# Kernel tuning notes

Hardware: AMD Instinct MI355X
Metric: run time of the kernel (lower is better)

Reference implementation:

```python
import jax, jax.numpy as jnp
import numpy as np

B, S, D, H = 4, 2048, 2048, 16
HD = D // H  # 128


def setup_inputs() -> dict:
    key = jax.random.key(0)
    k1, k2, k3 = jax.random.split(key, 3)
    sc = 1.0 / np.sqrt(D)
    return {
        "x": jax.random.normal(k1, (B, S, D), dtype=jnp.float32),
        "W_qkv": jax.random.normal(k2, (D, 3 * D), dtype=jnp.float32) * sc,
        "W_out": jax.random.normal(k3, (D, D), dtype=jnp.float32) * sc,
        "b_out": jnp.zeros((D,), dtype=jnp.float32),
    }


def _rotate_half(t):
    t1, t2 = jnp.split(t, 2, axis=-1)
    return jnp.concatenate([-t2, t1], axis=-1)


def reference(x, W_qkv, W_out, b_out):
    b, s, d = x.shape
    qkv = jnp.einsum('bsd,de->bse', x, W_qkv)  # fused QKV projection
    q, k, v = jnp.split(qkv, 3, axis=-1)
    # [b, h, s, hd]
    q = q.reshape(b, s, H, HD).transpose(0, 2, 1, 3)
    k = k.reshape(b, s, H, HD).transpose(0, 2, 1, 3)
    v = v.reshape(b, s, H, HD).transpose(0, 2, 1, 3)
    # RoPE (NeoX-style half-split), past_kv=None so positions = arange(s)
    pos = jnp.arange(s, dtype=jnp.float32)
    theta = 1.0 / (10000.0 ** (jnp.arange(0, HD, 2, dtype=jnp.float32) / HD))
    angles = pos[:, None] * theta[None, :]           # [s, hd/2]
    cos = jnp.concatenate([jnp.cos(angles)] * 2, -1)  # [s, hd] (repeat halves)
    sin = jnp.concatenate([jnp.sin(angles)] * 2, -1)
    cos = cos[None, None]  # [1,1,s,hd]
    sin = sin[None, None]
    q = q * cos + _rotate_half(q) * sin
    k = k * cos + _rotate_half(k) * sin
    # causal SDPA, scale = 1/sqrt(head_dim)
    scale = 1.0 / jnp.sqrt(jnp.asarray(HD, dtype=q.dtype))
    scores = jnp.einsum('bhqd,bhkd->bhqk', q, k) * scale
    causal = jnp.tril(jnp.ones((s, s), dtype=bool))
    scores = jnp.where(causal[None, None], scores, jnp.finfo(scores.dtype).min)
    attn = jax.nn.softmax(scores, axis=-1)
    out = jnp.einsum('bhqk,bhkd->bhqd', attn, v)
    out = out.transpose(0, 2, 1, 3).reshape(b, s, D)
    return jnp.einsum('bsd,de->bse', out, W_out) + b_out
```

## Files before the change

### kernel.cpp

```cpp
#include <hip/hip_runtime.h>

typedef unsigned short ushort_t;
typedef unsigned int u32;
typedef __attribute__((ext_vector_type(8))) short bf16x8;
typedef __attribute__((ext_vector_type(8))) unsigned short u16x8;
typedef __attribute__((ext_vector_type(4))) float f32x4;
typedef __attribute__((ext_vector_type(16))) float f32x16;

#define B_ 4
#define S_ 2048
#define D_ 2048
#define H_ 16
#define HD_ 128

__device__ __forceinline__ ushort_t f2bf(float f) {
  u32 x = __builtin_bit_cast(u32, f);
  x += 0x7fffu + ((x >> 16) & 1u);
  return (ushort_t)(x >> 16);
}
__device__ __forceinline__ float bf2f(ushort_t u) {
  u32 x = ((u32)u) << 16;
  return __builtin_bit_cast(float, x);
}

#define GLL16(srcp, ldsp)                                            \
  __builtin_amdgcn_global_load_lds(                                  \
      (const __attribute__((address_space(1))) u32*)(srcp),          \
      (__attribute__((address_space(3))) u32*)(ldsp), 16, 0, 0)

struct __align__(8) us4 { ushort_t x, y, z, w; };

__global__ void k_cvt_bf16(const float* __restrict__ in, ushort_t* __restrict__ out, int n) {
  int i = (blockIdx.x * 256 + threadIdx.x) * 4;
  if (i >= n) return;
  float4 v = *(const float4*)(in + i);
  us4 o;
  o.x = f2bf(v.x); o.y = f2bf(v.y); o.z = f2bf(v.z); o.w = f2bf(v.w);
  *(us4*)(out + i) = o;
}

__global__ void k_transpose_bf16(const float* __restrict__ in, ushort_t* __restrict__ out,
                                 int R, int C) {
  __shared__ float ld[32][33];
  int c0 = blockIdx.x * 32, r0 = blockIdx.y * 32;
  int tc = threadIdx.x & 31, tr = threadIdx.x >> 5;
#pragma unroll
  for (int i = 0; i < 4; ++i) {
    int r = tr + i * 8;
    ld[r][tc] = in[(size_t)(r0 + r) * C + c0 + tc];
  }
  __syncthreads();
#pragma unroll
  for (int i = 0; i < 4; ++i) {
    int r = tr + i * 8;
    out[(size_t)(c0 + r) * R + r0 + tc] = f2bf(ld[tc][r]);
  }
}

__global__ void k_rope_tables(float* __restrict__ cost, float* __restrict__ sint) {
  int i = blockIdx.x * 256 + threadIdx.x;
  int s = i >> 6, j = i & 63;
  double th = pow(10000.0, -(double)j / 64.0);
  double a = (double)s * th;
  cost[i] = (float)cos(a);
  sint[i] = (float)sin(a);
}

template <int MODE>
__global__ __launch_bounds__(512) void k_g8(const ushort_t* __restrict__ A,
                                            const ushort_t* __restrict__ Bt,
                                            void* __restrict__ Cout,
                                            const float* __restrict__ bias,
                                            ushort_t* __restrict__ VtB,
                                            int M, int N, int K) {
  __shared__ __attribute__((aligned(16))) ushort_t As[2][256 * 64];
  __shared__ __attribute__((aligned(16))) ushort_t Bs[2][256 * 64];
  const int tid = threadIdx.x;
  const int w = tid >> 6, l = tid & 63;
  const int l31 = l & 31, hl = l >> 5;
  const int wm = w >> 2, wn = w & 3;

  const int cpx = gridDim.x >> 3;
  const int bid = blockIdx.x;
  const int swzid = (bid & 7) * cpx + (bid >> 3);
  const int nbn = N >> 8;
  const size_t m0 = (size_t)(swzid / nbn) * 256;
  const size_t n0 = (size_t)(swzid % nbn) * 256;

  const size_t Kp = (size_t)K * 2;
  const char* Ab = (const char*)A + m0 * Kp;
  const char* Bb = (const char*)Bt + n0 * Kp;

  const int r0 = tid >> 3;
  const int ci16 = (tid & 7) * 16;
  const int sw0 = (((tid & 7) ^ (r0 & 7)) << 4);
  const int sw1 = (((tid & 7) ^ ((r0 + 64) & 7)) << 4);

#define STG_HALF(gbase, hrow, ldsbase, tcol)                                   \
  {                                                                            \
    GLL16((gbase) + (size_t)((hrow) + r0) * Kp + (tcol) + sw0,                 \
          (char*)(ldsbase) + ((hrow) + r0) * 128 + ci16);                      \
    GLL16((gbase) + (size_t)((hrow) + r0 + 64) * Kp + (tcol) + sw1,            \
          (char*)(ldsbase) + ((hrow) + r0 + 64) * 128 + ci16);                 \
  }

  f32x16 acc[4][2] = {};
  const int NI = K >> 7;

  const int arow = wm * 128 + l31;
  const int brow0 = wn * 64 + l31;

  STG_HALF(Ab, 0,   As[0], (size_t)0);
  STG_HALF(Ab, 128, As[0], (size_t)0);
  STG_HALF(Bb, 0,   Bs[0], (size_t)0);
  STG_HALF(Bb, 128, Bs[0], (size_t)0);
  STG_HALF(Bb, 0,   Bs[1], (size_t)128);
  STG_HALF(Bb, 128, Bs[1], (size_t)128);
  asm volatile("s_waitcnt vmcnt(4)");
  __builtin_amdgcn_sched_barrier(0);
  __builtin_amdgcn_s_barrier();

  for (int it = 0; it < NI; ++it) {
    const int t1 = 2 * it + 1;
    const bool more = (it + 1 < NI);
    const size_t cA1 = (size_t)t1 * 128;
    const size_t cT2 = (size_t)(t1 + 1) * 128;
    const size_t cT3 = (size_t)(t1 + 2) * 128;
    bf16x8 bq[2][4];
#pragma unroll
    for (int ph = 0; ph < 8; ++ph) {
      const int slot = ph >> 2;
      const int q = ph & 3;
      const char* Ac = (const char*)As[slot];
      const char* Bc = (const char*)Bs[slot];
      bf16x8 af[4];
      const int ar = arow + q * 32;
#pragma unroll
      for (int ks = 0; ks < 4; ++ks) {
        const int c = ks * 2 + hl;
        af[ks] = *(const bf16x8*)(Ac + ar * 128 + ((c ^ (ar & 7)) << 4));
      }
      if (q == 0) {
#pragma unroll
        for (int nt = 0; nt < 2; ++nt) {
          const int br = brow0 + nt * 32;
#pragma unroll
          for (int ks = 0; ks < 4; ++ks) {
            const int c = ks * 2 + hl;
            bq[nt][ks] = *(const bf16x8*)(Bc + br * 128 + ((c ^ (br & 7)) << 4));
          }
        }
      }
      if (ph == 0)      STG_HALF(Ab, 0,   As[1], cA1)
      else if (ph == 1) STG_HALF(Ab, 128, As[1], cA1)
      else if (ph == 2) { if (more) STG_HALF(Bb, 0,   Bs[0], cT2) }
      else if (ph == 3) { if (more) STG_HALF(Bb, 128, Bs[0], cT2) }
      else if (ph == 4) { if (more) STG_HALF(Ab, 0,   As[0], cT2) }
      else if (ph == 5) { if (more) STG_HALF(Ab, 128, As[0], cT2) }
      else if (ph == 6) { if (more) STG_HALF(Bb, 0,   Bs[1], cT3) }
      else              { if (more) STG_HALF(Bb, 128, Bs[1], cT3) }
      asm volatile("s_waitcnt lgkmcnt(0)");
      __builtin_amdgcn_sched_barrier(0);
      __builtin_amdgcn_s_setprio(1);
#pragma unroll
      for (int ks = 0; ks < 4; ++ks) {
        acc[q][0] = __builtin_amdgcn_mfma_f32_32x32x16_bf16(af[ks], bq[0][ks], acc[q][0], 0, 0, 0);
        acc[q][1] = __builtin_amdgcn_mfma_f32_32x32x16_bf16(af[ks], bq[1][ks], acc[q][1], 0, 0, 0);
      }
      __builtin_amdgcn_s_setprio(0);
      if (ph == 3) {
        if (more) asm volatile("s_waitcnt vmcnt(4)");
        else      asm volatile("s_waitcnt vmcnt(0)");
        __builtin_amdgcn_sched_barrier(0);
      } else if (ph == 7 && more) {
        asm volatile("s_waitcnt vmcnt(4)");
        __builtin_amdgcn_sched_barrier(0);
      }
      __builtin_amdgcn_s_barrier();
    }
  }

  if (MODE == 2) {
#pragma unroll
    for (int nt = 0; nt < 2; ++nt) {
      const size_t col = n0 + wn * 64 + nt * 32 + l31;
      const float bia = bias[col];
#pragma unroll
      for (int mt = 0; mt < 4; ++mt)
#pragma unroll
        for (int r = 0; r < 16; ++r) {
          const size_t row = m0 + wm * 128 + mt * 32 + (r & 3) + 8 * (r >> 2) + 4 * hl;
          ((float*)Cout)[row * N + col] = acc[mt][nt][r] + bia;
        }
    }
  } else {
    ushort_t* Qbase = (ushort_t*)Cout;
#pragma unroll
    for (int nt = 0; nt < 2; ++nt) {
      const int col = (int)n0 + wn * 64 + nt * 32 + l31;
      const int p3 = col >> 11, rem = col & 2047;
      const int h = rem >> 7, d = rem & 127;
      if (p3 < 2) {
        ushort_t* base = Qbase + (size_t)p3 * 16777216ull + (size_t)h * (S_ * HD_) + d;
#pragma unroll
        for (int mt = 0; mt < 4; ++mt)
#pragma unroll
          for (int r = 0; r < 16; ++r) {
            const int row = (int)m0 + wm * 128 + mt * 32 + (r & 3) + 8 * (r >> 2) + 4 * hl;
            const int b2 = row >> 11, s = row & 2047;
            base[(size_t)b2 * (H_ * S_ * HD_) + (size_t)s * HD_] = f2bf(acc[mt][nt][r]);
          }
      } else {
        ushort_t* baseV = VtB + ((size_t)h * HD_ + d) * S_;
#pragma unroll
        for (int mt = 0; mt < 4; ++mt)
#pragma unroll
          for (int r = 0; r < 16; ++r) {
            const int row = (int)m0 + wm * 128 + mt * 32 + (r & 3) + 8 * (r >> 2) + 4 * hl;
            const int b2 = row >> 11, s = row & 2047;
            baseV[(size_t)b2 * ((size_t)H_ * HD_ * S_) + s] = f2bf(acc[mt][nt][r]);
          }
      }
    }
  }
#undef STG_HALF
}

__global__ void k_rope2(ushort_t* __restrict__ Qr, ushort_t* __restrict__ Kr,
                        const float* __restrict__ cost, const float* __restrict__ sint,
                        float qs) {
  int s0 = blockIdx.x * 32, h = blockIdx.y, z = blockIdx.z;
  const bool isQ = (z < B_);
  const int b = isQ ? z : z - B_;
  const float sc = isQ ? qs : 1.0f;
  ushort_t* t8 = isQ ? Qr : Kr;
  int bh = b * H_ + h;
  const int t = threadIdx.x;
  const int sr = t >> 3, dj = (t & 7) * 8;
  const int s = s0 + sr;
  ushort_t* base = t8 + ((size_t)bh * S_ + s) * HD_;
  u16x8 lo = *(const u16x8*)(base + dj);
  u16x8 hi = *(const u16x8*)(base + 64 + dj);
  const float* cs = cost + s * 64 + dj;
  const float* sn = sint + s * 64 + dj;
  u16x8 olo, ohi;
#pragma unroll
  for (int j = 0; j < 8; ++j) {
    float fl = bf2f(lo[j]), fh = bf2f(hi[j]);
    float c = cs[j], sv = sn[j];
    olo[j] = f2bf((fl * c - fh * sv) * sc);
    ohi[j] = f2bf((fh * c + fl * sv) * sc);
  }
  *(u16x8*)(base + dj) = olo;
  *(u16x8*)(base + 64 + dj) = ohi;
}

__global__ __launch_bounds__(256, 2) void k_attn6(const ushort_t* __restrict__ Q,
                                                  const ushort_t* __restrict__ K,
                                                  const ushort_t* __restrict__ Vt,
                                                  ushort_t* __restrict__ O) {
  __shared__ __attribute__((aligned(16))) ushort_t Ks[2][64 * 128];
  __shared__ __attribute__((aligned(16))) ushort_t Vs[128 * 64];
  __shared__ __attribute__((aligned(16))) ushort_t Pl[8][16 * 72];

  const int id = blockIdx.x;
  const int work = (id & 7) * 128 + (id >> 3);
  const int bh = work >> 4;
  const int qt = 15 - (work & 15);
  const int b = bh >> 4, h = bh & 15;

  const int tid = threadIdx.x;
  const int w = tid >> 6, l = tid & 63;
  const int lr = l & 15, lg = l >> 4;
  const int qb = qt * 128 + w * 32;

  const ushort_t* Qp = Q + (size_t)bh * S_ * HD_;
  const char* Kpb = (const char*)(K + (size_t)bh * S_ * HD_);
  const char* Vpb = (const char*)(Vt + (size_t)bh * HD_ * S_);

  int kr[4], ksz[4], vr[4], vsz[4];
#pragma unroll
  for (int r = 0; r < 4; ++r) {
    int c = r * 256 + tid;
    kr[r] = c >> 4;
    ksz[r] = (((c & 15) ^ (kr[r] & 15)) << 4);
    vr[r] = c >> 3;
    vsz[r] = (((c & 7) ^ (vr[r] & 7)) << 4);
  }

#define STAGE_K(kb_, bufi)                                                       \
  {                                                                              \
    _Pragma("unroll") for (int r = 0; r < 4; ++r)                                \
        GLL16(Kpb + (size_t)((kb_) + kr[r]) * 256 + ksz[r],                      \
              (char*)Ks[bufi] + (size_t)(r * 256 + tid) * 16);                   \
  }
#define STAGE_V(kb_)                                                             \
  {                                                                              \
    _Pragma("unroll") for (int r = 0; r < 4; ++r)                                \
        GLL16(Vpb + (size_t)vr[r] * (S_ * 2) + (size_t)(kb_) * 2 + vsz[r],       \
              (char*)Vs + (size_t)(r * 256 + tid) * 16);                         \
  }

  bf16x8 qf[2][4];
#pragma unroll
  for (int f = 0; f < 2; ++f)
#pragma unroll
    for (int dw = 0; dw < 4; ++dw)
      qf[f][dw] = *(const bf16x8*)(Qp + (size_t)(qb + f * 16 + lr) * HD_ + dw * 32 + lg * 8);

  f32x4 oacc[2][8] = {};
  float lsum[2] = {0.f, 0.f};
  const int nkt = 2 * qt + 2;

  STAGE_K(0, 0);
  for (int kt = 0; kt < nkt; ++kt) {
    const int kb = kt * 64;
    const int cur = kt & 1;
    const bool morek = (kt + 1 < nkt);
    if (morek) STAGE_K(kb + 64, cur ^ 1);
    STAGE_V(kb);
    if (morek) asm volatile("s_waitcnt vmcnt(8)");
    else       asm volatile("s_waitcnt vmcnt(4)");
    __builtin_amdgcn_sched_barrier(0);
    __builtin_amdgcn_s_barrier();

    const bool live = (kb <= qb + 31);
    f32x4 st[2][4];
    if (live) {
      const char* Kc = (const char*)Ks[cur];
      __builtin_amdgcn_s_setprio(1);
#pragma unroll
      for (int t = 0; t < 4; ++t) {
        bf16x8 kf[4];
#pragma unroll
        for (int dw = 0; dw < 4; ++dw)
          kf[dw] = *(const bf16x8*)(Kc + (t * 16 + lr) * 256 + (((dw * 4 + lg) ^ lr) << 4));
        f32x4 a0 = {}, a1 = {};
#pragma unroll
        for (int dw = 0; dw < 4; ++dw) {
          a0 = __builtin_amdgcn_mfma_f32_16x16x32_bf16(kf[dw], qf[0][dw], a0, 0, 0, 0);
          a1 = __builtin_amdgcn_mfma_f32_16x16x32_bf16(kf[dw], qf[1][dw], a1, 0, 0, 0);
        }
        st[0][t] = a0;
        st[1][t] = a1;
      }
      __builtin_amdgcn_s_setprio(0);

#pragma unroll
      for (int f = 0; f < 2; ++f) {
        const int qg = qb + f * 16 + lr;
        const bool full = (kb + 63) <= (qb + f * 16);
        if (!full) {
#pragma unroll
          for (int t = 0; t < 4; ++t)
#pragma unroll
            for (int j = 0; j < 4; ++j) {
              int kg = kb + t * 16 + lg * 4 + j;
              st[f][t][j] = (kg > qg) ? -1e30f : st[f][t][j];
            }
        }
        float psum = 0.f;
        ushort_t* Pw = (ushort_t*)Pl[w * 2 + f];
#pragma unroll
        for (int t = 0; t < 4; ++t) {
          float p0 = exp2f(st[f][t][0]);
          float p1 = exp2f(st[f][t][1]);
          float p2 = exp2f(st[f][t][2]);
          float p3 = exp2f(st[f][t][3]);
          psum += (p0 + p1) + (p2 + p3);
          u32 pk0, pk1;
          asm("v_cvt_pk_bf16_f32 %0, %1, %2" : "=v"(pk0) : "v"(p0), "v"(p1));
          asm("v_cvt_pk_bf16_f32 %0, %1, %2" : "=v"(pk1) : "v"(p2), "v"(p3));
          *(u32*)&Pw[lr * 72 + t * 16 + lg * 4] = pk0;
          *(u32*)&Pw[lr * 72 + t * 16 + lg * 4 + 2] = pk1;
        }
        lsum[f] += psum;
      }
    }
    if (morek) asm volatile("s_waitcnt vmcnt(4)");
    else       asm volatile("s_waitcnt vmcnt(0)");
    __builtin_amdgcn_sched_barrier(0);
    __builtin_amdgcn_s_barrier();

    if (live) {
      __builtin_amdgcn_s_setprio(1);
#pragma unroll
      for (int kw = 0; kw < 2; ++kw) {
        bf16x8 pa0 = *(const bf16x8*)&Pl[w * 2 + 0][lr * 72 + kw * 32 + lg * 8];
        bf16x8 pa1 = *(const bf16x8*)&Pl[w * 2 + 1][lr * 72 + kw * 32 + lg * 8];
#pragma unroll
        for (int dt = 0; dt < 8; ++dt) {
          bf16x8 vf = *(const bf16x8*)((const char*)Vs + (dt * 16 + lr) * 128 +
                                       (((kw * 4 + lg) ^ (lr & 7)) << 4));
          oacc[0][dt] = __builtin_amdgcn_mfma_f32_16x16x32_bf16(pa0, vf, oacc[0][dt], 0, 0, 0);
          oacc[1][dt] = __builtin_amdgcn_mfma_f32_16x16x32_bf16(pa1, vf, oacc[1][dt], 0, 0, 0);
        }
      }
      __builtin_amdgcn_s_setprio(0);
    }
    __builtin_amdgcn_s_barrier();
  }

#pragma unroll
  for (int f = 0; f < 2; ++f) {
    lsum[f] += __shfl_xor(lsum[f], 16, 64);
    lsum[f] += __shfl_xor(lsum[f], 32, 64);
    float l0 = __shfl(lsum[f], lg * 4 + 0, 64);
    float l1 = __shfl(lsum[f], lg * 4 + 1, 64);
    float l2 = __shfl(lsum[f], lg * 4 + 2, 64);
    float l3 = __shfl(lsum[f], lg * 4 + 3, 64);
    float i0 = 1.f / l0, i1 = 1.f / l1, i2 = 1.f / l2, i3 = 1.f / l3;
    ushort_t* Op = O + (size_t)(b * S_ + qb + f * 16) * D_ + h * HD_;
#pragma unroll
    for (int dt = 0; dt < 8; ++dt) {
      Op[(size_t)(lg * 4 + 0) * D_ + dt * 16 + lr] = f2bf(oacc[f][dt][0] * i0);
      Op[(size_t)(lg * 4 + 1) * D_ + dt * 16 + lr] = f2bf(oacc[f][dt][1] * i1);
      Op[(size_t)(lg * 4 + 2) * D_ + dt * 16 + lr] = f2bf(oacc[f][dt][2] * i2);
      Op[(size_t)(lg * 4 + 3) * D_ + dt * 16 + lr] = f2bf(oacc[f][dt][3] * i3);
    }
  }
#undef STAGE_K
#undef STAGE_V
}

extern "C" void kernel_launch(void* const* d_in, const int* in_sizes, int n_in,
                              void* d_out, int out_size, void* d_ws, size_t ws_size,
                              hipStream_t stream) {
  const float* x = (const float*)d_in[0];
  const float* Wqkv = (const float*)d_in[1];
  const float* Wout = (const float*)d_in[2];
  const float* bout = (const float*)d_in[3];
  char* ws = (char*)d_ws;

  ushort_t* xb  = (ushort_t*)(ws + 0);
  ushort_t* Wqt = (ushort_t*)(ws + 33554432ull);
  ushort_t* Qr  = (ushort_t*)(ws + 58720256ull);
  ushort_t* Kr  = (ushort_t*)(ws + 92274688ull);
  ushort_t* Vr  = (ushort_t*)(ws + 125829120ull);
  ushort_t* Vt  = (ushort_t*)(ws + 159383552ull);
  float* cost   = (float*)(ws + 192937984ull);
  float* sint   = (float*)(ws + 193462272ull);

  const int M = B_ * S_;
  const float kSc = 0.08838834764831845f * 1.4426950408889634f;

  k_cvt_bf16<<<dim3((M * D_) / 4 / 256), 256, 0, stream>>>(x, xb, M * D_);
  k_transpose_bf16<<<dim3(3 * D_ / 32, D_ / 32), 256, 0, stream>>>(Wqkv, Wqt, D_, 3 * D_);
  k_rope_tables<<<dim3(S_ * 64 / 256), 256, 0, stream>>>(cost, sint);

  k_g8<1><<<dim3((M / 256) * (3 * D_ / 256)), 512, 0, stream>>>(
      xb, Wqt, Qr, nullptr, Vt, M, 3 * D_, D_);

  k_rope2<<<dim3(S_ / 32, H_, 2 * B_), 256, 0, stream>>>(Qr, Kr, cost, sint, kSc);

  k_transpose_bf16<<<dim3(D_ / 32, D_ / 32), 256, 0, stream>>>(Wout, Vr, D_, D_);

  k_attn6<<<dim3((S_ / 128) * B_ * H_), 256, 0, stream>>>(Qr, Kr, Vt, xb );

  k_g8<2><<<dim3((M / 256) * (D_ / 256)), 512, 0, stream>>>(
      xb, Vr, d_out, bout, nullptr, M, D_, D_);
}
```

Baseline: 486.3 us.

## Double-buffer V with K and drop mid-iteration barrier in attention

```diff
diff --git a/kernel.cpp b/kernel.cpp
--- a/kernel.cpp
+++ b/kernel.cpp
@@ -255,13 +255,13 @@
   *(u16x8*)(base + 64 + dj) = ohi;
 }
 
-__global__ __launch_bounds__(256, 2) void k_attn6(const ushort_t* __restrict__ Q,
+__global__ __launch_bounds__(256, 2) void k_attn9(const ushort_t* __restrict__ Q,
                                                   const ushort_t* __restrict__ K,
                                                   const ushort_t* __restrict__ Vt,
                                                   ushort_t* __restrict__ O) {
   __shared__ __attribute__((aligned(16))) ushort_t Ks[2][64 * 128];
-  __shared__ __attribute__((aligned(16))) ushort_t Vs[128 * 64];
-  __shared__ __attribute__((aligned(16))) ushort_t Pl[8][16 * 72];
+  __shared__ __attribute__((aligned(16))) ushort_t Vs[2][128 * 64];
+  __shared__ __attribute__((aligned(16))) ushort_t Pl[8][1024];
 
   const int id = blockIdx.x;
   const int work = (id & 7) * 128 + (id >> 3);
@@ -278,28 +278,25 @@
   const char* Kpb = (const char*)(K + (size_t)bh * S_ * HD_);
   const char* Vpb = (const char*)(Vt + (size_t)bh * HD_ * S_);
 
-  int kr[4], ksz[4], vr[4], vsz[4];
+  int kr[4], ksz[4], vrw[4], vsz[4];
 #pragma unroll
   for (int r = 0; r < 4; ++r) {
     int c = r * 256 + tid;
     kr[r] = c >> 4;
     ksz[r] = (((c & 15) ^ (kr[r] & 15)) << 4);
-    vr[r] = c >> 3;
-    vsz[r] = (((c & 7) ^ (vr[r] & 7)) << 4);
-  }
-
-#define STAGE_K(kb_, bufi)                                                       \
+    vrw[r] = c >> 3;
+    vsz[r] = (((c & 7) ^ (vrw[r] & 7)) << 4);
+  }
+
+#define STAGE_KV(kb_, bufi)                                                      \
   {                                                                              \
+    _Pragma("unroll") for (int r = 0; r < 4; ++r)                                \
+        GLL16(Vpb + (size_t)vrw[r] * (S_ * 2) + (size_t)(kb_) * 2 + vsz[r],      \
+              (char*)Vs[bufi] + (size_t)(r * 256 + tid) * 16);                   \
     _Pragma("unroll") for (int r = 0; r < 4; ++r)                                \
         GLL16(Kpb + (size_t)((kb_) + kr[r]) * 256 + ksz[r],                      \
               (char*)Ks[bufi] + (size_t)(r * 256 + tid) * 16);                   \
   }
-#define STAGE_V(kb_)                                                             \
-  {                                                                              \
-    _Pragma("unroll") for (int r = 0; r < 4; ++r)                                \
-        GLL16(Vpb + (size_t)vr[r] * (S_ * 2) + (size_t)(kb_) * 2 + vsz[r],       \
-              (char*)Vs + (size_t)(r * 256 + tid) * 16);                         \
-  }
 
   bf16x8 qf[2][4];
 #pragma unroll
@@ -312,22 +309,25 @@
   float lsum[2] = {0.f, 0.f};
   const int nkt = 2 * qt + 2;
 
-  STAGE_K(0, 0);
+  STAGE_KV(0, 0);
   for (int kt = 0; kt < nkt; ++kt) {
     const int kb = kt * 64;
     const int cur = kt & 1;
     const bool morek = (kt + 1 < nkt);
-    if (morek) STAGE_K(kb + 64, cur ^ 1);
-    STAGE_V(kb);
-    if (morek) asm volatile("s_waitcnt vmcnt(8)");
-    else       asm volatile("s_waitcnt vmcnt(4)");
+    if (morek) {
+      STAGE_KV(kb + 64, cur ^ 1);
+      asm volatile("s_waitcnt vmcnt(8)");
+    } else {
+      asm volatile("s_waitcnt vmcnt(0)");
+    }
     __builtin_amdgcn_sched_barrier(0);
     __builtin_amdgcn_s_barrier();
 
     const bool live = (kb <= qb + 31);
-    f32x4 st[2][4];
     if (live) {
       const char* Kc = (const char*)Ks[cur];
+      const char* Vc = (const char*)Vs[cur];
+      f32x4 st[2][4];
       __builtin_amdgcn_s_setprio(1);
 #pragma unroll
       for (int t = 0; t < 4; ++t) {
@@ -360,7 +360,7 @@
             }
         }
         float psum = 0.f;
-        ushort_t* Pw = (ushort_t*)Pl[w * 2 + f];
+        char* Pw = (char*)Pl + (w * 2 + f) * 2048;
 #pragma unroll
         for (int t = 0; t < 4; ++t) {
           float p0 = exp2f(st[f][t][0]);
@@ -371,26 +371,24 @@
           u32 pk0, pk1;
           asm("v_cvt_pk_bf16_f32 %0, %1, %2" : "=v"(pk0) : "v"(p0), "v"(p1));
           asm("v_cvt_pk_bf16_f32 %0, %1, %2" : "=v"(pk1) : "v"(p2), "v"(p3));
-          *(u32*)&Pw[lr * 72 + t * 16 + lg * 4] = pk0;
-          *(u32*)&Pw[lr * 72 + t * 16 + lg * 4 + 2] = pk1;
+          const int byt = lr * 128 + (((2 * t + (lg >> 1)) ^ (lr & 7)) << 4) + ((lg & 1) << 3);
+          *(u32*)(Pw + byt) = pk0;
+          *(u32*)(Pw + byt + 4) = pk1;
         }
         lsum[f] += psum;
       }
-    }
-    if (morek) asm volatile("s_waitcnt vmcnt(4)");
-    else       asm volatile("s_waitcnt vmcnt(0)");
-    __builtin_amdgcn_sched_barrier(0);
-    __builtin_amdgcn_s_barrier();
-
-    if (live) {
+
+      const char* Pw0 = (const char*)Pl + (w * 2) * 2048;
+      const char* Pw1 = (const char*)Pl + (w * 2 + 1) * 2048;
       __builtin_amdgcn_s_setprio(1);
 #pragma unroll
       for (int kw = 0; kw < 2; ++kw) {
-        bf16x8 pa0 = *(const bf16x8*)&Pl[w * 2 + 0][lr * 72 + kw * 32 + lg * 8];
-        bf16x8 pa1 = *(const bf16x8*)&Pl[w * 2 + 1][lr * 72 + kw * 32 + lg * 8];
+        const int pbyt = lr * 128 + (((kw * 4 + lg) ^ (lr & 7)) << 4);
+        bf16x8 pa0 = *(const bf16x8*)(Pw0 + pbyt);
+        bf16x8 pa1 = *(const bf16x8*)(Pw1 + pbyt);
 #pragma unroll
         for (int dt = 0; dt < 8; ++dt) {
-          bf16x8 vf = *(const bf16x8*)((const char*)Vs + (dt * 16 + lr) * 128 +
+          bf16x8 vf = *(const bf16x8*)(Vc + (dt * 16 + lr) * 128 +
                                        (((kw * 4 + lg) ^ (lr & 7)) << 4));
           oacc[0][dt] = __builtin_amdgcn_mfma_f32_16x16x32_bf16(pa0, vf, oacc[0][dt], 0, 0, 0);
           oacc[1][dt] = __builtin_amdgcn_mfma_f32_16x16x32_bf16(pa1, vf, oacc[1][dt], 0, 0, 0);
@@ -419,8 +417,7 @@
       Op[(size_t)(lg * 4 + 3) * D_ + dt * 16 + lr] = f2bf(oacc[f][dt][3] * i3);
     }
   }
-#undef STAGE_K
-#undef STAGE_V
+#undef STAGE_KV
 }
 
 extern "C" void kernel_launch(void* const* d_in, const int* in_sizes, int n_in,
@@ -455,7 +452,7 @@
 
   k_transpose_bf16<<<dim3(D_ / 32, D_ / 32), 256, 0, stream>>>(Wout, Vr, D_, D_);
 
-  k_attn6<<<dim3((S_ / 128) * B_ * H_), 256, 0, stream>>>(Qr, Kr, Vt, xb );
+  k_attn9<<<dim3((S_ / 128) * B_ * H_), 256, 0, stream>>>(Qr, Kr, Vt, xb );
 
   k_g8<2><<<dim3((M / 256) * (D_ / 256)), 512, 0, stream>>>(
       xb, Vr, d_out, bout, nullptr, M, D_, D_);
```

Measured after the change: 484.0 us (median of 2 runs). Within noise of the previous version (-0.5%).
